# Kernel tuning notes

Hardware: AMD Instinct MI355X
Metric: run time of the kernel (lower is better)

The kernel has to match this reference:

```python
import jax, jax.numpy as jnp
import numpy as np

B, T, I, H, V, E = 512, 256, 256, 1024, 1024, 8
FUT = 64


def _lstm_cell(x_t, h, c, Wih, Whh, b):
    # PyTorch gate order: i, f, g, o. b = b_ih + b_hh (mathematically identical).
    z = x_t @ Wih.T + h @ Whh.T + b  # [B, 4H]
    i, f, g, o = jnp.split(z, 4, axis=-1)
    i = jax.nn.sigmoid(i)
    f = jax.nn.sigmoid(f)
    g = jnp.tanh(g)
    o = jax.nn.sigmoid(o)
    c_new = f * c + i * g
    h_new = o * jnp.tanh(c_new)
    return h_new, c_new


def setup_inputs() -> dict:
    key = jax.random.key(0)
    ks = jax.random.split(key, 10)
    s = 0.02
    return {
        "x_hist": jax.random.normal(ks[0], (B, T, I), jnp.float32),
        "enc_Wih": jax.random.normal(ks[1], (4 * H, I), jnp.float32) * s,
        "enc_Whh": jax.random.normal(ks[2], (4 * H, H), jnp.float32) * s,
        "enc_b": jnp.zeros((4 * H,), jnp.float32),
        "embed_W": jax.random.normal(ks[3], (V, E), jnp.float32),
        "dec_Wih": jax.random.normal(ks[4], (4 * H, E), jnp.float32) * s,
        "dec_Whh": jax.random.normal(ks[5], (4 * H, H), jnp.float32) * s,
        "dec_b": jnp.zeros((4 * H,), jnp.float32),
        "fc_W": jax.random.normal(ks[6], (V, H), jnp.float32) * s,
        "fc_b": jnp.zeros((V,), jnp.float32),
        "future_len": FUT,
    }


def reference(x_hist, enc_Wih, enc_Whh, enc_b, embed_W, dec_Wih, dec_Whh,
              dec_b, fc_W, fc_b, future_len):
    bsz = x_hist.shape[0]
    h0 = jnp.zeros((bsz, enc_Whh.shape[1]), x_hist.dtype)
    c0 = jnp.zeros_like(h0)

    # Encoder LSTM over history (batch_first): scan over time.
    def enc_step(carry, x_t):
        h, c = carry
        h, c = _lstm_cell(x_t, h, c, enc_Wih, enc_Whh, enc_b)
        return (h, c), None

    (h, c), _ = jax.lax.scan(enc_step, (h0, c0), jnp.swapaxes(x_hist, 0, 1))

    y0 = jnp.zeros((bsz,), jnp.int32)

    def dec_step(carry, _):
        h, c, y_prev = carry
        x = embed_W[y_prev]                       # [B, E] embedding lookup
        h, c = _lstm_cell(x, h, c, dec_Wih, dec_Whh, dec_b)
        logits = h @ fc_W.T + fc_b                # [B, V]
        y = jnp.argmax(logits, axis=1).astype(jnp.int32)
        return (h, c, y), logits

    _, logits = jax.lax.scan(dec_step, (h, c, y0), None, length=future_len)
    return jnp.swapaxes(logits, 0, 1)             # [B, future_len, V]
```

## Files before the change

### kernel.cpp

```cpp
#include <hip/hip_runtime.h>
#include <cmath>

typedef __attribute__((ext_vector_type(8))) short short8;
typedef __attribute__((ext_vector_type(4))) float f32x4;

#define B_SZ 512
#define T_SZ 256
#define I_SZ 256
#define H_SZ 1024
#define V_SZ 1024
#define E_SZ 8
#define FUT 64

#define KVE 3840
#define KVD 3328
#define KVF 3072
#define APE 2560
#define APD 2176

static __device__ __forceinline__ ushort f2bf(float v) {
    uint32_t u = __float_as_uint(v);
    uint32_t r = (u + 0x7fffu + ((u >> 16) & 1u)) >> 16;
    return (ushort)r;
}
static __device__ __forceinline__ float bf2f(ushort b) {
    return __uint_as_float(((uint32_t)b) << 16);
}
static __device__ __forceinline__ uint32_t fmono(float f) {
    uint32_t u = __float_as_uint(f);
    return (u & 0x80000000u) ? ~u : (u | 0x80000000u);
}

#define GLD16(gp, lp)                                                          \
    __builtin_amdgcn_global_load_lds(                                         \
        (const __attribute__((address_space(1))) void*)(gp),                  \
        (__attribute__((address_space(3))) void*)(lp), 16, 0, 0)

template<int MFR, int NFR, int NTPX, int NK, int T1, int T2,
         int O0, int O1, int O2, bool GATES>
__global__ __launch_bounds__(256) void gemm_step(
    const ushort* __restrict__ A, int astr,
    const ushort* __restrict__ W, int kv,
    const float* __restrict__ bias,
    float* __restrict__ c,
    ushort* __restrict__ hdest, int ldh,
    const float* __restrict__ xsrc, ushort* __restrict__ xdest,
    float* __restrict__ out, int ldo,
    unsigned long long* __restrict__ keys)
{
    constexpr int ABUF = MFR * 2048;
    constexpr int WBUF = NFR * 2048;
    __shared__ __align__(16) ushort lds[4 * (ABUF + WBUF)];

    const int tid = threadIdx.x;
    const int lane = tid & 63;
    const int wid = tid >> 6;
    const int wm = wid >> 1, wn = wid & 1;
    const int l15 = lane & 15, lq = lane >> 4;
    const int l7 = lane & 7, l3 = lane >> 3;

    const int flat = blockIdx.x;
    const int xcd = flat & 7, slot = flat >> 3;
    const int n_tile = xcd * NTPX + (slot % NTPX);
    const int m_tile = slot / NTPX;
    const int m0 = m_tile * (MFR * 32);
    const int n0 = n_tile * (NFR * 32);

    f32x4 acc[MFR][NFR];
#pragma unroll
    for (int m = 0; m < MFR; ++m)
#pragma unroll
        for (int n = 0; n < NFR; ++n) { f32x4 z = {0.f, 0.f, 0.f, 0.f}; acc[m][n] = z; }

    auto STAGE = [&](int p, int bufi) {
        const int off = p < T1 ? O0 : (p < T2 ? O1 : O2);
        const int kc = p * 64;
        ushort* ab = &lds[bufi * ABUF];
        ushort* wb = &lds[4 * ABUF + bufi * WBUF];
#pragma unroll
        for (int i = 0; i < MFR; ++i) {
            const int rowg = (i * 4 + wid) * 8;
            const int row = rowg + l3;
            GLD16(A + (size_t)(m0 + row) * astr + kc + off + ((l7 ^ l3) * 8),
                  ab + rowg * 64);
        }
#pragma unroll
        for (int i = 0; i < NFR; ++i) {
            const int rowg = (i * 4 + wid) * 8;
            const int row = rowg + l3;
            GLD16(W + (size_t)(n0 + row) * kv + kc + ((l7 ^ l3) * 8),
                  wb + rowg * 64);
        }
    };
    auto COMPUTE = [&](int bufi) {
        const ushort* ab = &lds[bufi * ABUF];
        const ushort* wb = &lds[4 * ABUF + bufi * WBUF];
#pragma unroll
        for (int kk = 0; kk < 2; ++kk) {
            short8 af[MFR], wf[NFR];
#pragma unroll
            for (int m = 0; m < MFR; ++m) {
                const int row = wm * (MFR * 16) + m * 16 + l15;
                af[m] = *(const short8*)
                    &ab[row * 64 + (((kk * 4 + lq) ^ (row & 7)) * 8)];
            }
#pragma unroll
            for (int n = 0; n < NFR; ++n) {
                const int row = wn * (NFR * 16) + n * 16 + l15;
                wf[n] = *(const short8*)
                    &wb[row * 64 + (((kk * 4 + lq) ^ (row & 7)) * 8)];
            }
#pragma unroll
            for (int m = 0; m < MFR; ++m)
#pragma unroll
                for (int n = 0; n < NFR; ++n)
                    acc[m][n] = __builtin_amdgcn_mfma_f32_16x16x32_bf16(
                        af[m], wf[n], acc[m][n], 0, 0, 0);
        }
    };

    STAGE(0, 0);
    if (NK > 1) STAGE(1, 1);
    if (NK > 2) STAGE(2, 2);
#pragma unroll 1
    for (int p0 = 0; p0 < NK; p0 += 4) {
#pragma unroll
        for (int j = 0; j < 4; ++j) {
            const int p = p0 + j;
            if (p < NK) {
                if (p + 2 < NK) {
                    if constexpr (MFR + NFR == 4)
                        asm volatile("s_waitcnt vmcnt(8)" ::: "memory");
                    else
                        asm volatile("s_waitcnt vmcnt(4)" ::: "memory");
                } else if (p + 1 < NK) {
                    if constexpr (MFR + NFR == 4)
                        asm volatile("s_waitcnt vmcnt(4)" ::: "memory");
                    else
                        asm volatile("s_waitcnt vmcnt(2)" ::: "memory");
                } else {
                    asm volatile("s_waitcnt vmcnt(0)" ::: "memory");
                }
                __builtin_amdgcn_s_barrier();
                if (p + 3 < NK) STAGE(p + 3, (j + 3) & 3);
                COMPUTE(j);
            }
        }
    }

    if constexpr (GATES) {
        float* zs = (float*)&lds[0];
        __syncthreads();
#pragma unroll
        for (int m = 0; m < MFR; ++m)
#pragma unroll
            for (int n = 0; n < NFR; ++n)
#pragma unroll
                for (int r = 0; r < 4; ++r)
                    zs[(wm * 32 + m * 16 + lq * 4 + r) * 65 +
                       wn * 32 + n * 16 + l15] = acc[m][n][r];
        __syncthreads();

        const int row = tid & 63;
        const int jl0 = (tid >> 6) * 4;
        const int grow = m0 + row;
        const int jg = n_tile * 16 + jl0;
        const f32x4 bi4 = *(const f32x4*)&bias[n0 + jl0];
        const f32x4 bf4 = *(const f32x4*)&bias[n0 + 16 + jl0];
        const f32x4 bg4 = *(const f32x4*)&bias[n0 + 32 + jl0];
        const f32x4 bo4 = *(const f32x4*)&bias[n0 + 48 + jl0];
        f32x4 cv = *(f32x4*)&c[(size_t)grow * H_SZ + jg];
        ushort hh[4], hl[4];
#pragma unroll
        for (int jj = 0; jj < 4; ++jj) {
            const float zi = zs[row * 65 + jl0 + jj] + bi4[jj];
            const float zf = zs[row * 65 + 16 + jl0 + jj] + bf4[jj];
            const float zg = zs[row * 65 + 32 + jl0 + jj] + bg4[jj];
            const float zo = zs[row * 65 + 48 + jl0 + jj] + bo4[jj];
            const float ig = 1.f / (1.f + expf(-zi));
            const float fg = 1.f / (1.f + expf(-zf));
            const float gg = tanhf(zg);
            const float og = 1.f / (1.f + expf(-zo));
            const float cn = fg * cv[jj] + ig * gg;
            cv[jj] = cn;
            const float hv = og * tanhf(cn);
            hh[jj] = f2bf(hv);
            hl[jj] = f2bf(hv - bf2f(hh[jj]));
        }
        *(f32x4*)&c[(size_t)grow * H_SZ + jg] = cv;
        ushort* hd = hdest + (size_t)grow * ldh + jg;
        uint hv2[2], lv2[2];
        hv2[0] = (uint)hh[0] | ((uint)hh[1] << 16);
        hv2[1] = (uint)hh[2] | ((uint)hh[3] << 16);
        lv2[0] = (uint)hl[0] | ((uint)hl[1] << 16);
        lv2[1] = (uint)hl[2] | ((uint)hl[3] << 16);
        *(uint*)&hd[0] = hv2[0];
        *(uint*)&hd[2] = hv2[1];
        *(uint*)&hd[1024] = lv2[0];
        *(uint*)&hd[1026] = lv2[1];

        if (xdest) {
            const int idx = flat * 256 + tid;
            const int b = idx >> 8, i = idx & 255;
            const float v = xsrc[(size_t)b * (T_SZ * I_SZ) + i];
            const ushort hi = f2bf(v), lo = f2bf(v - bf2f(hi));
            xdest[(size_t)b * APE + i] = hi;
            xdest[(size_t)b * APE + 256 + i] = lo;
        }
    } else {
        float vals[4];
        const int col = n0 + wn * 16 + l15;
        const float bv = bias[col];
#pragma unroll
        for (int r = 0; r < 4; ++r) {
            const int row = m0 + wm * 16 + lq * 4 + r;
            vals[r] = acc[0][0][r] + bv;
            out[(size_t)row * ldo + col] = vals[r];
        }
        if (keys) {
            float* zs = (float*)&lds[0];
            __syncthreads();
#pragma unroll
            for (int r = 0; r < 4; ++r)
                zs[(wm * 16 + lq * 4 + r) * 33 + wn * 16 + l15] = vals[r];
            __syncthreads();
            if (tid < 32) {
                const int row = tid;
                float best = zs[row * 33];
                int bc = 0;
#pragma unroll
                for (int cc = 1; cc < 32; ++cc) {
                    const float x = zs[row * 33 + cc];
                    if (x > best) { best = x; bc = cc; }
                }
                const unsigned long long key =
                    ((unsigned long long)fmono(best) << 32) |
                    (unsigned long long)(V_SZ - 1 - (n0 + bc));
                atomicMax(&keys[m0 + row], key);
            }
        }
    }
}

__global__ __launch_bounds__(256) void gather_embed(
    unsigned long long* __restrict__ keys,
    const float* __restrict__ embed_W,
    ushort* __restrict__ xdest)
{
    const int idx = blockIdx.x * 256 + threadIdx.x;
    const int b = idx >> 3, e = idx & 7;
    const unsigned long long key = keys[b];
    const int yb = V_SZ - 1 - (int)(key & 0xffffffffu);
    const float v = embed_W[(size_t)yb * E_SZ + e];
    const ushort hi = f2bf(v), lo = f2bf(v - bf2f(hi));
    ushort* xd = xdest + (size_t)b * APD;
    xd[e] = hi;
    xd[8 + e] = hi;
    xd[16 + e] = lo;
    if (e == 0) keys[b] = 0ull;
}

__global__ void pack_enc(const float* __restrict__ Wih, const float* __restrict__ Whh,
                         const float* __restrict__ b, ushort* __restrict__ Wp,
                         float* __restrict__ bp)
{
    const int k = blockIdx.x * 256 + threadIdx.x;
    const int np = blockIdx.y;
    const int orig = ((np >> 4) & 3) * H_SZ + (np >> 6) * 16 + (np & 15);
    float v; bool lo = false;
    if (k < 256)        v = Wih[(size_t)orig * I_SZ + k];
    else if (k < 512) { v = Wih[(size_t)orig * I_SZ + k - 256]; lo = true; }
    else if (k < 768)   v = Wih[(size_t)orig * I_SZ + k - 512];
    else if (k < 1792)  v = Whh[(size_t)orig * H_SZ + k - 768];
    else if (k < 2816) { v = Whh[(size_t)orig * H_SZ + k - 1792]; lo = true; }
    else                v = Whh[(size_t)orig * H_SZ + k - 2816];
    const ushort hi = f2bf(v);
    Wp[(size_t)np * KVE + k] = lo ? f2bf(v - bf2f(hi)) : hi;
    if (k == 0) bp[np] = b[orig];
}

__global__ void pack_dec(const float* __restrict__ Wih, const float* __restrict__ Whh,
                         const float* __restrict__ b, ushort* __restrict__ Wp,
                         float* __restrict__ bp)
{
    const int k = blockIdx.x * 256 + threadIdx.x;
    const int np = blockIdx.y;
    const int orig = ((np >> 4) & 3) * H_SZ + (np >> 6) * 16 + (np & 15);
    float v = 0.f; bool lo = false; bool zero = false;
    if (k < 8)            v = Wih[(size_t)orig * E_SZ + k];
    else if (k < 16)    { v = Wih[(size_t)orig * E_SZ + k - 8]; lo = true; }
    else if (k < 24)      v = Wih[(size_t)orig * E_SZ + k - 16];
    else if (k < 128)     zero = true;
    else if (k < 1152)    v = Whh[(size_t)orig * H_SZ + k - 128];
    else if (k < 2176)  { v = Whh[(size_t)orig * H_SZ + k - 1152]; lo = true; }
    else if (k < 3200)    v = Whh[(size_t)orig * H_SZ + k - 2176];
    else                  zero = true;
    ushort w = 0;
    if (!zero) { const ushort hi = f2bf(v); w = lo ? f2bf(v - bf2f(hi)) : hi; }
    Wp[(size_t)np * KVD + k] = w;
    if (k == 0) bp[np] = b[orig];
}

__global__ void pack_fc(const float* __restrict__ W, ushort* __restrict__ Wp)
{
    const int k = blockIdx.x * 256 + threadIdx.x;
    const int np = blockIdx.y;
    float v; bool lo = false;
    if (k < 1024)       v = W[(size_t)np * H_SZ + k];
    else if (k < 2048) { v = W[(size_t)np * H_SZ + k - 1024]; lo = true; }
    else                v = W[(size_t)np * H_SZ + k - 2048];
    const ushort hi = f2bf(v);
    Wp[(size_t)np * KVF + k] = lo ? f2bf(v - bf2f(hi)) : hi;
}

__global__ void init_all(const float* __restrict__ x0,
                         const float* __restrict__ embed_W,
                         float* __restrict__ c,
                         ushort* __restrict__ Aenc0,
                         ushort* __restrict__ Adec0,
                         ushort* __restrict__ Adec1,
                         unsigned long long* __restrict__ keys)
{
    const int idx = blockIdx.x * 256 + threadIdx.x;
    {
        const int b = idx >> 11, k = idx & 2047;
        Aenc0[(size_t)b * APE + 512 + k] = 0;
    }
    if (idx < B_SZ * H_SZ) c[idx] = 0.f;
    if (idx < B_SZ) keys[idx] = 0ull;
    if (idx < B_SZ * I_SZ) {
        const int b = idx >> 8, i = idx & 255;
        const float v = x0[(size_t)b * (T_SZ * I_SZ) + i];
        const ushort hi = f2bf(v), lo = f2bf(v - bf2f(hi));
        Aenc0[(size_t)b * APE + i] = hi;
        Aenc0[(size_t)b * APE + 256 + i] = lo;
    }
    if (idx < B_SZ * 104) {
        const int b = idx / 104, col = 24 + idx % 104;
        Adec0[(size_t)b * APD + col] = 0;
        Adec1[(size_t)b * APD + col] = 0;
    }
    if (idx < B_SZ * 24) {
        const int b = idx / 24, col = idx % 24;
        float v;
        if (col < 8)       v = embed_W[col];
        else if (col < 16) v = embed_W[col - 8];
        else               v = embed_W[col - 16];
        const ushort hi = f2bf(v);
        Adec0[(size_t)b * APD + col] = (col < 16) ? hi : f2bf(v - bf2f(hi));
    }
}

extern "C" void kernel_launch(void* const* d_in, const int* in_sizes, int n_in,
                              void* d_out, int out_size, void* d_ws, size_t ws_size,
                              hipStream_t stream)
{
    const float* x_hist  = (const float*)d_in[0];
    const float* enc_Wih = (const float*)d_in[1];
    const float* enc_Whh = (const float*)d_in[2];
    const float* enc_b   = (const float*)d_in[3];
    const float* embed_W = (const float*)d_in[4];
    const float* dec_Wih = (const float*)d_in[5];
    const float* dec_Whh = (const float*)d_in[6];
    const float* dec_b   = (const float*)d_in[7];
    const float* fc_W    = (const float*)d_in[8];
    const float* fc_b    = (const float*)d_in[9];
    float* out = (float*)d_out;

    char* p = (char*)d_ws;
    auto alloc = [&](size_t bytes) {
        char* r = p;
        p += (bytes + 255) & ~(size_t)255;
        return r;
    };
    ushort* W_enc  = (ushort*)alloc((size_t)4096 * KVE * 2);
    ushort* W_dec  = (ushort*)alloc((size_t)4096 * KVD * 2);
    ushort* W_fc   = (ushort*)alloc((size_t)1024 * KVF * 2);
    ushort* A_enc0 = (ushort*)alloc((size_t)B_SZ * APE * 2);
    ushort* A_enc1 = (ushort*)alloc((size_t)B_SZ * APE * 2);
    ushort* A_dec0 = (ushort*)alloc((size_t)B_SZ * APD * 2);
    ushort* A_dec1 = (ushort*)alloc((size_t)B_SZ * APD * 2);
    float*  cbuf   = (float*)alloc((size_t)B_SZ * H_SZ * 4);
    float*  bpe    = (float*)alloc(4096 * 4);
    float*  bpd    = (float*)alloc(4096 * 4);
    unsigned long long* keys = (unsigned long long*)alloc(B_SZ * 8);

    const dim3 blk(256);
    hipLaunchKernelGGL(pack_enc, dim3(15, 4096), blk, 0, stream, enc_Wih, enc_Whh, enc_b, W_enc, bpe);
    hipLaunchKernelGGL(pack_dec, dim3(13, 4096), blk, 0, stream, dec_Wih, dec_Whh, dec_b, W_dec, bpd);
    hipLaunchKernelGGL(pack_fc,  dim3(12, 1024), blk, 0, stream, fc_W, W_fc);
    hipLaunchKernelGGL(init_all, dim3(4096), blk, 0, stream, x_hist, embed_W, cbuf, A_enc0, A_dec0, A_dec1, keys);

    ushort* Ae[2] = {A_enc0, A_enc1};
    ushort* Ad[2] = {A_dec0, A_dec1};

    for (int t = 0; t < T_SZ; ++t) {
        ushort* hdst; int ldh; const float* xs; ushort* xd;
        if (t < T_SZ - 1) {
            hdst = Ae[(t + 1) & 1] + 512; ldh = APE;
            xs = x_hist + (size_t)(t + 1) * I_SZ;
            xd = Ae[(t + 1) & 1];
        } else {
            hdst = Ad[0] + 128; ldh = APD;
            xs = nullptr; xd = nullptr;
        }
        hipLaunchKernelGGL((gemm_step<2, 2, 8, 60, 4, 28, 0, -256, -1280, true>),
                           dim3(512), blk, 0, stream,
                           Ae[t & 1], APE, W_enc, KVE, bpe, cbuf,
                           hdst, ldh, xs, xd, (float*)nullptr, 0,
                           (unsigned long long*)nullptr);
    }

    for (int t = 0; t < FUT; ++t) {
        hipLaunchKernelGGL((gemm_step<2, 2, 8, 50, 18, 50, 0, -1024, -1024, true>),
                           dim3(512), blk, 0, stream,
                           Ad[t & 1], APD, W_dec, KVD, bpd, cbuf,
                           Ad[(t + 1) & 1] + 128, APD,
                           (const float*)nullptr, (ushort*)nullptr,
                           (float*)nullptr, 0,
                           (unsigned long long*)nullptr);
        float* logits = out + (size_t)t * V_SZ;
        hipLaunchKernelGGL((gemm_step<1, 1, 4, 48, 16, 48, 128, -896, -896, false>),
                           dim3(512), blk, 0, stream,
                           Ad[(t + 1) & 1], APD, W_fc, KVF, fc_b,
                           (float*)nullptr, (ushort*)nullptr, 0,
                           (const float*)nullptr, (ushort*)nullptr,
                           logits, FUT * V_SZ, keys);
        hipLaunchKernelGGL(gather_embed, dim3(16), blk, 0, stream,
                           keys, embed_W, Ad[(t + 1) & 1]);
    }
}
```

Baseline: 10.02 ms.

## Reuse staged activation tile for hi and lo weight halves in split-bf16 GEMM

Reorders the packed weight layouts so the hi and lo bf16 weight halves of each 64-wide K chunk sit next to each other. The GEMM stages one A tile against a 128-wide weight tile, so the activation chunk is loaded into LDS once and used for both halves. This removes the duplicated activation loads from the 3-pass split-precision product, and the decoder weight padding shrinks as well. The pipeline changes from 4-deep to 3-deep buffering with new wait counts, which risks less latency hiding and makes the offset and packing consistency delicate.

```diff
diff --git a/kernel.cpp b/kernel.cpp
--- a/kernel.cpp
+++ b/kernel.cpp
@@ -13,7 +13,7 @@
 #define FUT 64
 
 #define KVE 3840
-#define KVD 3328
+#define KVD 3200
 #define KVF 3072
 #define APE 2560
 #define APD 2176
@@ -30,14 +30,23 @@
     uint32_t u = __float_as_uint(f);
     return (u & 0x80000000u) ? ~u : (u | 0x80000000u);
 }
+template<int N>
+static __device__ __forceinline__ void waitvm() {
+    if constexpr (N == 0)      asm volatile("s_waitcnt vmcnt(0)" ::: "memory");
+    else if constexpr (N == 2) asm volatile("s_waitcnt vmcnt(2)" ::: "memory");
+    else if constexpr (N == 3) asm volatile("s_waitcnt vmcnt(3)" ::: "memory");
+    else if constexpr (N == 4) asm volatile("s_waitcnt vmcnt(4)" ::: "memory");
+    else if constexpr (N == 6) asm volatile("s_waitcnt vmcnt(6)" ::: "memory");
+}
 
 #define GLD16(gp, lp)                                                          \
     __builtin_amdgcn_global_load_lds(                                         \
         (const __attribute__((address_space(1))) void*)(gp),                  \
         (__attribute__((address_space(3))) void*)(lp), 16, 0, 0)
 
-template<int MFR, int NFR, int NTPX, int NK, int T1, int T2,
-         int O0, int O1, int O2, bool GATES>
+template<int MFR, int NFR, int NTPX,
+         int NKP, int PT1, int PO0, int PO1,
+         int NKS, int ST1, int SO0, int SO1, bool GATES>
 __global__ __launch_bounds__(256) void gemm_step(
     const ushort* __restrict__ A, int astr,
     const ushort* __restrict__ W, int kv,
@@ -49,8 +58,8 @@
     unsigned long long* __restrict__ keys)
 {
     constexpr int ABUF = MFR * 2048;
-    constexpr int WBUF = NFR * 2048;
-    __shared__ __align__(16) ushort lds[4 * (ABUF + WBUF)];
+    constexpr int WBUF = NFR * 4096;
+    __shared__ __align__(16) ushort lds[3 * ABUF + 3 * WBUF];
 
     const int tid = threadIdx.x;
     const int lane = tid & 63;
@@ -72,32 +81,46 @@
 #pragma unroll
         for (int n = 0; n < NFR; ++n) { f32x4 z = {0.f, 0.f, 0.f, 0.f}; acc[m][n] = z; }
 
-    auto STAGE = [&](int p, int bufi) {
-        const int off = p < T1 ? O0 : (p < T2 ? O1 : O2);
-        const int kc = p * 64;
+    auto stageA = [&](int kcA, int bufi) {
         ushort* ab = &lds[bufi * ABUF];
-        ushort* wb = &lds[4 * ABUF + bufi * WBUF];
 #pragma unroll
         for (int i = 0; i < MFR; ++i) {
             const int rowg = (i * 4 + wid) * 8;
             const int row = rowg + l3;
-            GLD16(A + (size_t)(m0 + row) * astr + kc + off + ((l7 ^ l3) * 8),
+            GLD16(A + (size_t)(m0 + row) * astr + kcA + ((l7 ^ (row & 7)) * 8),
                   ab + rowg * 64);
         }
+    };
+    auto stageP = [&](int p, int bufi) {
+        stageA(p * 64 + (p < PT1 ? PO0 : PO1), bufi);
+        const int kcW = p * 128;
+        ushort* wb = &lds[3 * ABUF + bufi * WBUF];
+#pragma unroll
+        for (int i = 0; i < 2 * NFR; ++i) {
+            const int rowg = (i * 4 + wid) * 4;
+            const int row = rowg + lq;
+            GLD16(W + (size_t)(n0 + row) * kv + kcW + ((l15 ^ (row & 15)) * 8),
+                  wb + rowg * 128);
+        }
+    };
+    auto stageS = [&](int s, int bufi) {
+        stageA(s * 64 + (s < ST1 ? SO0 : SO1), bufi);
+        const int kcW = NKP * 128 + s * 64;
+        ushort* wb = &lds[3 * ABUF + bufi * WBUF];
 #pragma unroll
         for (int i = 0; i < NFR; ++i) {
             const int rowg = (i * 4 + wid) * 8;
             const int row = rowg + l3;
-            GLD16(W + (size_t)(n0 + row) * kv + kc + ((l7 ^ l3) * 8),
+            GLD16(W + (size_t)(n0 + row) * kv + kcW + ((l7 ^ (row & 7)) * 8),
                   wb + rowg * 64);
         }
     };
-    auto COMPUTE = [&](int bufi) {
+    auto compP = [&](int bufi) {
         const ushort* ab = &lds[bufi * ABUF];
-        const ushort* wb = &lds[4 * ABUF + bufi * WBUF];
+        const ushort* wb = &lds[3 * ABUF + bufi * WBUF];
 #pragma unroll
         for (int kk = 0; kk < 2; ++kk) {
-            short8 af[MFR], wf[NFR];
+            short8 af[MFR];
 #pragma unroll
             for (int m = 0; m < MFR; ++m) {
                 const int row = wm * (MFR * 16) + m * 16 + l15;
@@ -105,6 +128,36 @@
                     &ab[row * 64 + (((kk * 4 + lq) ^ (row & 7)) * 8)];
             }
 #pragma unroll
+            for (int sub = 0; sub < 2; ++sub) {
+                short8 wf[NFR];
+#pragma unroll
+                for (int n = 0; n < NFR; ++n) {
+                    const int row = wn * (NFR * 16) + n * 16 + l15;
+                    wf[n] = *(const short8*)
+                        &wb[row * 128 + (((sub * 8 + kk * 4 + lq) ^ (row & 15)) * 8)];
+                }
+#pragma unroll
+                for (int m = 0; m < MFR; ++m)
+#pragma unroll
+                    for (int n = 0; n < NFR; ++n)
+                        acc[m][n] = __builtin_amdgcn_mfma_f32_16x16x32_bf16(
+                            af[m], wf[n], acc[m][n], 0, 0, 0);
+            }
+        }
+    };
+    auto compS = [&](int bufi) {
+        const ushort* ab = &lds[bufi * ABUF];
+        const ushort* wb = &lds[3 * ABUF + bufi * WBUF];
+#pragma unroll
+        for (int kk = 0; kk < 2; ++kk) {
+            short8 af[MFR], wf[NFR];
+#pragma unroll
+            for (int m = 0; m < MFR; ++m) {
+                const int row = wm * (MFR * 16) + m * 16 + l15;
+                af[m] = *(const short8*)
+                    &ab[row * 64 + (((kk * 4 + lq) ^ (row & 7)) * 8)];
+            }
+#pragma unroll
             for (int n = 0; n < NFR; ++n) {
                 const int row = wn * (NFR * 16) + n * 16 + l15;
                 wf[n] = *(const short8*)
@@ -119,31 +172,26 @@
         }
     };
 
-    STAGE(0, 0);
-    if (NK > 1) STAGE(1, 1);
-    if (NK > 2) STAGE(2, 2);
+    auto STG = [&](int i, int b) { if (i < NKP) stageP(i, b); else stageS(i - NKP, b); };
+
+    constexpr int NT = NKP + NKS;
+    constexpr int GP = MFR + 2 * NFR;
+    constexpr int GS = MFR + NFR;
+
+    STG(0, 0);
+    STG(1, 1);
 #pragma unroll 1
-    for (int p0 = 0; p0 < NK; p0 += 4) {
-#pragma unroll
-        for (int j = 0; j < 4; ++j) {
-            const int p = p0 + j;
-            if (p < NK) {
-                if (p + 2 < NK) {
-                    if constexpr (MFR + NFR == 4)
-                        asm volatile("s_waitcnt vmcnt(8)" ::: "memory");
-                    else
-                        asm volatile("s_waitcnt vmcnt(4)" ::: "memory");
-                } else if (p + 1 < NK) {
-                    if constexpr (MFR + NFR == 4)
-                        asm volatile("s_waitcnt vmcnt(4)" ::: "memory");
-                    else
-                        asm volatile("s_waitcnt vmcnt(2)" ::: "memory");
-                } else {
-                    asm volatile("s_waitcnt vmcnt(0)" ::: "memory");
-                }
+    for (int i0 = 0; i0 < NT; i0 += 3) {
+#pragma unroll
+        for (int j = 0; j < 3; ++j) {
+            const int i = i0 + j;
+            if (i < NT) {
+                if (i + 1 < NKP)     waitvm<GP>();
+                else if (i + 1 < NT) waitvm<GS>();
+                else                 waitvm<0>();
                 __builtin_amdgcn_s_barrier();
-                if (p + 3 < NK) STAGE(p + 3, (j + 3) & 3);
-                COMPUTE(j);
+                if (i + 2 < NT) STG(i + 2, (j + 2) % 3);
+                if (i < NKP) compP(j); else compS(j);
             }
         }
     }
@@ -268,12 +316,16 @@
     const int np = blockIdx.y;
     const int orig = ((np >> 4) & 3) * H_SZ + (np >> 6) * 16 + (np & 15);
     float v; bool lo = false;
-    if (k < 256)        v = Wih[(size_t)orig * I_SZ + k];
-    else if (k < 512) { v = Wih[(size_t)orig * I_SZ + k - 256]; lo = true; }
-    else if (k < 768)   v = Wih[(size_t)orig * I_SZ + k - 512];
-    else if (k < 1792)  v = Whh[(size_t)orig * H_SZ + k - 768];
-    else if (k < 2816) { v = Whh[(size_t)orig * H_SZ + k - 1792]; lo = true; }
-    else                v = Whh[(size_t)orig * H_SZ + k - 2816];
+    if (k < 2560) {
+        const int p = k >> 7, cc = k & 63;
+        lo = (k >> 6) & 1;
+        v = (p < 4) ? Wih[(size_t)orig * I_SZ + p * 64 + cc]
+                    : Whh[(size_t)orig * H_SZ + (p - 4) * 64 + cc];
+    } else {
+        const int s = (k - 2560) >> 6, cc = k & 63;
+        v = (s < 4) ? Wih[(size_t)orig * I_SZ + s * 64 + cc]
+                    : Whh[(size_t)orig * H_SZ + (s - 4) * 64 + cc];
+    }
     const ushort hi = f2bf(v);
     Wp[(size_t)np * KVE + k] = lo ? f2bf(v - bf2f(hi)) : hi;
     if (k == 0) bp[np] = b[orig];
@@ -285,16 +337,25 @@
 {
     const int k = blockIdx.x * 256 + threadIdx.x;
     const int np = blockIdx.y;
+    if (k >= KVD) return;
     const int orig = ((np >> 4) & 3) * H_SZ + (np >> 6) * 16 + (np & 15);
     float v = 0.f; bool lo = false; bool zero = false;
-    if (k < 8)            v = Wih[(size_t)orig * E_SZ + k];
-    else if (k < 16)    { v = Wih[(size_t)orig * E_SZ + k - 8]; lo = true; }
-    else if (k < 24)      v = Wih[(size_t)orig * E_SZ + k - 16];
-    else if (k < 128)     zero = true;
-    else if (k < 1152)    v = Whh[(size_t)orig * H_SZ + k - 128];
-    else if (k < 2176)  { v = Whh[(size_t)orig * H_SZ + k - 1152]; lo = true; }
-    else if (k < 3200)    v = Whh[(size_t)orig * H_SZ + k - 2176];
-    else                  zero = true;
+    if (k < 2048) {
+        const int p = k >> 7, cc = k & 63;
+        lo = (k >> 6) & 1;
+        v = Whh[(size_t)orig * H_SZ + p * 64 + cc];
+    } else {
+        const int s = (k - 2048) >> 6, cc = k & 63;
+        if (s < 2) {
+            const int j = s * 64 + cc;
+            if (j < 8)       v = Wih[(size_t)orig * E_SZ + j];
+            else if (j < 16) { v = Wih[(size_t)orig * E_SZ + j - 8]; lo = true; }
+            else if (j < 24) v = Wih[(size_t)orig * E_SZ + j - 16];
+            else             zero = true;
+        } else {
+            v = Whh[(size_t)orig * H_SZ + (s - 2) * 64 + cc];
+        }
+    }
     ushort w = 0;
     if (!zero) { const ushort hi = f2bf(v); w = lo ? f2bf(v - bf2f(hi)) : hi; }
     Wp[(size_t)np * KVD + k] = w;
@@ -306,9 +367,14 @@
     const int k = blockIdx.x * 256 + threadIdx.x;
     const int np = blockIdx.y;
     float v; bool lo = false;
-    if (k < 1024)       v = W[(size_t)np * H_SZ + k];
-    else if (k < 2048) { v = W[(size_t)np * H_SZ + k - 1024]; lo = true; }
-    else                v = W[(size_t)np * H_SZ + k - 2048];
+    if (k < 2048) {
+        const int p = k >> 7, cc = k & 63;
+        lo = (k >> 6) & 1;
+        v = W[(size_t)np * H_SZ + p * 64 + cc];
+    } else {
+        const int s = (k - 2048) >> 6, cc = k & 63;
+        v = W[(size_t)np * H_SZ + s * 64 + cc];
+    }
     const ushort hi = f2bf(v);
     Wp[(size_t)np * KVF + k] = lo ? f2bf(v - bf2f(hi)) : hi;
 }
@@ -404,7 +470,7 @@
             hdst = Ad[0] + 128; ldh = APD;
             xs = nullptr; xd = nullptr;
         }
-        hipLaunchKernelGGL((gemm_step<2, 2, 8, 60, 4, 28, 0, -256, -1280, true>),
+        hipLaunchKernelGGL((gemm_step<2, 2, 8, 20, 4, 0, 256, 20, 4, 256, 1280, true>),
                            dim3(512), blk, 0, stream,
                            Ae[t & 1], APE, W_enc, KVE, bpe, cbuf,
                            hdst, ldh, xs, xd, (float*)nullptr, 0,
@@ -412,7 +478,7 @@
     }
 
     for (int t = 0; t < FUT; ++t) {
-        hipLaunchKernelGGL((gemm_step<2, 2, 8, 50, 18, 50, 0, -1024, -1024, true>),
+        hipLaunchKernelGGL((gemm_step<2, 2, 8, 16, 16, 128, 128, 18, 2, 0, 1024, true>),
                            dim3(512), blk, 0, stream,
                            Ad[t & 1], APD, W_dec, KVD, bpd, cbuf,
                            Ad[(t + 1) & 1] + 128, APD,
@@ -420,7 +486,7 @@
                            (float*)nullptr, 0,
                            (unsigned long long*)nullptr);
         float* logits = out + (size_t)t * V_SZ;
-        hipLaunchKernelGGL((gemm_step<1, 1, 4, 48, 16, 48, 128, -896, -896, false>),
+        hipLaunchKernelGGL((gemm_step<1, 1, 4, 16, 16, 128, 128, 16, 16, 1152, 1152, false>),
                            dim3(512), blk, 0, stream,
                            Ad[(t + 1) & 1], APD, W_fc, KVF, fc_b,
                            (float*)nullptr, (ushort*)nullptr, 0,
```

New measurement: 9.829 ms (median of 2 runs). About the same (-1.9%).
